# Optimization experiments

Hardware: AMD Instinct MI355X
Metric: run time of the kernel (lower is better)

Reference implementation:

```python
import jax, jax.numpy as jnp
import numpy as np

D_MODEL = 1024
ED = 2048          # d_inner = 2 * d_model
N = 16             # d_state
DT_RANK = 64
K = 4              # d_conv
BETA = 0.6
ALPHA = 1.0
B_SZ, L = 1, 2048


def setup_inputs() -> dict:
    key = jax.random.key(0)
    ks = jax.random.split(key, 9)
    s = 0.02
    x = jax.random.normal(ks[0], (B_SZ, L, D_MODEL), jnp.float32)
    W_in = jax.random.normal(ks[1], (2 * ED, D_MODEL), jnp.float32) * s
    conv_w = jax.random.normal(ks[2], (ED, K), jnp.float32) * s
    conv_b = jax.random.normal(ks[3], (ED,), jnp.float32) * s
    W_x = jax.random.normal(ks[4], (DT_RANK + 2 * N, ED), jnp.float32) * s
    dt_std = DT_RANK ** -0.5
    W_dt = jax.random.uniform(ks[5], (ED, DT_RANK), jnp.float32, -dt_std, dt_std)
    # dt bias init: inverse-softplus of dt in [dt_min, dt_max]
    dt = jnp.exp(jax.random.uniform(ks[6], (ED,), jnp.float32)
                 * (np.log(0.1) - np.log(0.001)) + np.log(0.001))
    dt = jnp.clip(dt, 1e-4)
    b_dt = dt + jnp.log(-jnp.expm1(-dt))
    A_log = jnp.log(jnp.tile(jnp.arange(1, N + 1, dtype=jnp.float32), (ED, 1)))
    D = jnp.ones((ED,), jnp.float32)
    W_out = jax.random.normal(ks[7], (D_MODEL, ED), jnp.float32) * s
    return {"x": x, "W_in": W_in, "conv_w": conv_w, "conv_b": conv_b,
            "W_x": W_x, "W_dt": W_dt, "b_dt": b_dt, "A_log": A_log,
            "D": D, "W_out": W_out}


def _depthwise_causal_conv(xc, conv_w, conv_b):
    # xc: (B, L, ED); torch Conv1d(groups=ED, padding=K-1)[..., :L] == causal conv
    lhs = jnp.transpose(xc, (0, 2, 1))                       # (B, ED, L)
    lhs = jnp.pad(lhs, ((0, 0), (0, 0), (K - 1, 0)))
    out = jax.lax.conv_general_dilated(lhs, conv_w[:, None, :], (1,), 'VALID',
                                       feature_group_count=ED)  # (B, ED, L)
    return jnp.transpose(out, (0, 2, 1)) + conv_b


def _ssm_momentum(xc, W_x, W_dt, b_dt, A_log, D):
    A = -jnp.exp(A_log)                                      # (ED, N)
    dBC = xc @ W_x.T                                         # (B, L, dt_rank + 2N)
    delta, Bm, Cm = jnp.split(dBC, [DT_RANK, DT_RANK + N], axis=-1)
    delta = jax.nn.softplus(delta @ W_dt.T + b_dt)           # (B, L, ED)
    deltaA = jnp.exp(delta[..., None] * A)                   # (B, L, ED, N)
    u = ALPHA * delta[..., None] * Bm[:, :, None, :] * xc[..., None]  # (B, L, ED, N)

    def step(carry, inp):
        h, v = carry
        dA_t, u_t = inp
        v = BETA * v + u_t
        h = dA_t * h + v
        return (h, v), h

    h0 = jnp.zeros((xc.shape[0], ED, N), xc.dtype)
    _, hs = jax.lax.scan(step, (h0, h0),
                         (jnp.moveaxis(deltaA, 1, 0), jnp.moveaxis(u, 1, 0)))
    y = jnp.einsum('lben,bln->ble', hs, Cm)                  # (B, L, ED)
    return y + D * xc


def reference(x, W_in, conv_w, conv_b, W_x, W_dt, b_dt, A_log, D, W_out):
    xz = x @ W_in.T                                          # (B, L, 2*ED)
    xc, z = jnp.split(xz, 2, axis=-1)
    xc = jax.nn.silu(_depthwise_causal_conv(xc, conv_w, conv_b))
    y = _ssm_momentum(xc, W_x, W_dt, b_dt, A_log, D)
    return (y * jax.nn.silu(z)) @ W_out.T                    # (B, L, d_model)
```

## Files before the change

### kernel.cpp

```cpp
#include <hip/hip_runtime.h>
#include <hip/hip_bf16.h>
#include <math.h>

#define L 2048
#define DM 1024
#define ED 2048
#define NST 16
#define DTR 64
#define BETA 0.6f
#define NCHUNK 64
#define LCH 32
#define SPLITS 16
#define SPLIT4 4

typedef __bf16 bf16_t;
typedef __bf16 bf16x8 __attribute__((ext_vector_type(8)));
typedef __bf16 bf16x4 __attribute__((ext_vector_type(4)));
typedef float  floatx4 __attribute__((ext_vector_type(4)));


__global__ void k_fill(float* __restrict__ p, float v, int n) {
    int i = blockIdx.x * 256 + threadIdx.x;
    if (i < n) p[i] = v;
}

__global__ void k_cvt_all(const float4* __restrict__ sx, bf16x4* __restrict__ dx,
                          const float4* __restrict__ s1, bf16x4* __restrict__ d1,
                          const float4* __restrict__ s2, bf16x4* __restrict__ d2,
                          const float4* __restrict__ s3, bf16x4* __restrict__ d3,
                          const float4* __restrict__ s4, bf16x4* __restrict__ d4) {
    int i = blockIdx.x * 256 + threadIdx.x;
    const float4* s; bf16x4* d; int off;
    if (i < 524288)        { s = sx; d = dx; off = 0; }
    else if (i < 1572864)  { s = s1; d = d1; off = 524288; }
    else if (i < 1622016)  { s = s2; d = d2; off = 1572864; }
    else if (i < 1654784)  { s = s3; d = d3; off = 1622016; }
    else                   { s = s4; d = d4; off = 1654784; }
    int j = i - off;
    float4 f = s[j];
    bf16x4 o;
    o[0] = (bf16_t)f.x; o[1] = (bf16_t)f.y; o[2] = (bf16_t)f.z; o[3] = (bf16_t)f.w;
    d[j] = o;
}

template<int EPI, bool GUARD>
__global__ __launch_bounds__(256)
void k_gemm_bt(const bf16_t* __restrict__ X, const bf16_t* __restrict__ W,
               float* __restrict__ C, int M, int N, int K, int ldc, int ksz,
               const float* __restrict__ bias) {
    __shared__ bf16_t As[128 * 32];
    __shared__ bf16_t Bs[128 * 32];
    const int tid  = threadIdx.x;
    const int bx   = blockIdx.x, by = blockIdx.y;
    const int kbase = blockIdx.z * ksz;
    if (EPI != 2) C += (size_t)blockIdx.z * M * ldc;
    const int wave = tid >> 6, lane = tid & 63;
    const int wm   = (wave >> 1) * 64;
    const int wn   = (wave & 1) * 64;
    const int quad = lane >> 4, l16 = lane & 15;

    floatx4 acc[4][4];
#pragma unroll
    for (int i = 0; i < 4; i++)
#pragma unroll
        for (int j = 0; j < 4; j++)
            acc[i][j] = (floatx4){0.f, 0.f, 0.f, 0.f};

    for (int kt = kbase; kt < kbase + ksz; kt += 32) {
        if (GUARD) {
#pragma unroll
            for (int p = 0; p < 2; p++) {
                int e = p * 2048 + tid * 8;
                int r = e >> 5, c = e & 31;
                int arow = by * 128 + r;
                *(float4*)(&As[r * 32 + c]) =
                    *(const float4*)(&X[(size_t)arow * K + kt + c]);
                int brow = bx * 128 + r;
                float4 bv = make_float4(0.f, 0.f, 0.f, 0.f);
                if (brow < N) bv = *(const float4*)(&W[(size_t)brow * K + kt + c]);
                *(float4*)(&Bs[r * 32 + c]) = bv;
            }
        } else {
#pragma unroll
            for (int p = 0; p < 2; p++) {
                int e = p * 2048 + tid * 8;
                int r = e >> 5, c = e & 31;
                __builtin_amdgcn_global_load_lds(
                    (const __attribute__((address_space(1))) void*)&X[(size_t)(by * 128 + r) * K + kt + c],
                    (__attribute__((address_space(3))) void*)&As[e], 16, 0, 0);
                __builtin_amdgcn_global_load_lds(
                    (const __attribute__((address_space(1))) void*)&W[(size_t)(bx * 128 + r) * K + kt + c],
                    (__attribute__((address_space(3))) void*)&Bs[e], 16, 0, 0);
            }
        }
        __syncthreads();

        bf16x8 af[4], bfr[4];
#pragma unroll
        for (int mt = 0; mt < 4; mt++)
            af[mt] = *(const bf16x8*)(&As[(wm + mt * 16 + l16) * 32 + quad * 8]);
#pragma unroll
        for (int nt = 0; nt < 4; nt++)
            bfr[nt] = *(const bf16x8*)(&Bs[(wn + nt * 16 + l16) * 32 + quad * 8]);
#pragma unroll
        for (int mt = 0; mt < 4; mt++)
#pragma unroll
            for (int nt = 0; nt < 4; nt++)
                acc[mt][nt] = __builtin_amdgcn_mfma_f32_16x16x32_bf16(
                    af[mt], bfr[nt], acc[mt][nt], 0, 0, 0);
        __syncthreads();
    }

#pragma unroll
    for (int mt = 0; mt < 4; mt++) {
#pragma unroll
        for (int nt = 0; nt < 4; nt++) {
            int col = bx * 128 + wn + nt * 16 + l16;
            if (!GUARD || col < N) {
#pragma unroll
                for (int r4 = 0; r4 < 4; r4++) {
                    int row = by * 128 + wm + mt * 16 + quad * 4 + r4;
                    float v = acc[mt][nt][r4];
                    if (EPI == 1) {
                        v += bias[col];
                        v = (v > 20.f) ? v : log1pf(__expf(v));
                    }
                    if (EPI == 2) {
                        unsafeAtomicAdd(&C[(size_t)row * ldc + col], v);
                    } else {
                        C[(size_t)row * ldc + col] = v;
                    }
                }
            }
        }
    }
}

__global__ void k_conv_silu(const float* __restrict__ xz,
                            const float* __restrict__ conv_w,
                            const float* __restrict__ conv_b,
                            float* __restrict__ xc, bf16_t* __restrict__ xc_bf) {
    int idx = blockIdx.x * 256 + threadIdx.x;
    int e = idx & (ED - 1);
    int t = idx >> 11;
    float w0 = conv_w[e * 4 + 0], w1 = conv_w[e * 4 + 1];
    float w2 = conv_w[e * 4 + 2], w3 = conv_w[e * 4 + 3];
    const float* col = xz + e;
    float acc = conv_b[e];
    if (t >= 3) acc += w0 * col[(size_t)(t - 3) * 4096];
    if (t >= 2) acc += w1 * col[(size_t)(t - 2) * 4096];
    if (t >= 1) acc += w2 * col[(size_t)(t - 1) * 4096];
    acc += w3 * col[(size_t)t * 4096];
    float s = acc / (1.f + __expf(-acc));
    xc[idx] = s;
    xc_bf[idx] = (bf16_t)s;
}

__global__ void k_red2(const float* __restrict__ part, float* __restrict__ dBC,
                       bf16_t* __restrict__ dly) {
    int idx = blockIdx.x * 256 + threadIdx.x;
    int t = idx / 96, c = idx - t * 96;
    float s = 0.f;
#pragma unroll
    for (int sp = 0; sp < SPLITS; sp++) s += part[(size_t)sp * L * 96 + idx];
    dBC[idx] = s;
    if (c < 64) dly[t * 64 + c] = (bf16_t)s;
}


__global__ __launch_bounds__(256)
void k_scan_p1(const float* __restrict__ delta, const float* __restrict__ xc,
               const float* __restrict__ dBC, const float* __restrict__ A_log,
               float4* __restrict__ summ) {
    const int chunk = blockIdx.x >> 3;
    const int e = (blockIdx.x & 7) * 256 + threadIdx.x;
    float A[NST];
#pragma unroll
    for (int n = 0; n < NST; n++) A[n] = -__expf(A_log[e * NST + n]);
    float h[NST], v[NST], p[NST], q[NST];
#pragma unroll
    for (int n = 0; n < NST; n++) { h[n] = 0.f; v[n] = 0.f; p[n] = 1.f; q[n] = 0.f; }
    float bp = 1.f;
    const int t0 = chunk * LCH;
    for (int i = 0; i < LCH; i++) {
        int t = t0 + i;
        float d   = delta[(size_t)t * ED + e];
        float xcv = xc[(size_t)t * ED + e];
        float du  = d * xcv;
        bp *= BETA;
        const float* Bp = &dBC[t * 96 + 64];
#pragma unroll
        for (int n = 0; n < NST; n++) {
            float a = __expf(d * A[n]);
            v[n] = BETA * v[n] + du * Bp[n];
            h[n] = a * h[n] + v[n];
            p[n] *= a;
            q[n] = a * q[n] + bp;
        }
    }
#pragma unroll
    for (int n = 0; n < NST; n++)
        summ[((size_t)n * NCHUNK + chunk) * ED + e] = make_float4(h[n], v[n], p[n], q[n]);
}

__global__ void k_combine(float4* __restrict__ summ) {
    int tid = blockIdx.x * 256 + threadIdx.x;
    int n = tid >> 11, e = tid & (ED - 1);
    float2* s2 = (float2*)summ;
    float h = 0.f, v = 0.f;
    const float bl = 7.9586611e-8f;
#pragma unroll 8
    for (int c = 0; c < NCHUNK; c++) {
        size_t idx = ((size_t)n * NCHUNK + c) * ED + e;
        float4 f = summ[idx];
        s2[idx * 2] = make_float2(h, v);
        float hn = f.z * h + f.w * v + f.x;
        v = bl * v + f.y;
        h = hn;
    }
}

__global__ __launch_bounds__(256)
void k_scan_p2(const float* __restrict__ delta, const float* __restrict__ xc,
               const float* __restrict__ dBC, const float* __restrict__ A_log,
               const float4* __restrict__ summ, const float* __restrict__ Dvec,
               const float* __restrict__ xz, bf16_t* __restrict__ g) {
    const int chunk = blockIdx.x >> 3;
    const int e = (blockIdx.x & 7) * 256 + threadIdx.x;
    float A[NST];
#pragma unroll
    for (int n = 0; n < NST; n++) A[n] = -__expf(A_log[e * NST + n]);
    float h[NST], v[NST];
    const float2* s2 = (const float2*)summ;
#pragma unroll
    for (int n = 0; n < NST; n++) {
        float2 s = s2[(((size_t)n * NCHUNK + chunk) * ED + e) * 2];
        h[n] = s.x; v[n] = s.y;
    }
    const float De = Dvec[e];
    const int t0 = chunk * LCH;
    for (int i = 0; i < LCH; i++) {
        int t = t0 + i;
        float d   = delta[(size_t)t * ED + e];
        float xcv = xc[(size_t)t * ED + e];
        float du  = d * xcv;
        const float* Bp = &dBC[t * 96 + 64];
        const float* Cp = &dBC[t * 96 + 80];
        float yacc = 0.f;
#pragma unroll
        for (int n = 0; n < NST; n++) {
            float a = __expf(d * A[n]);
            v[n] = BETA * v[n] + du * Bp[n];
            h[n] = a * h[n] + v[n];
            yacc += Cp[n] * h[n];
        }
        float z = xz[(size_t)t * 4096 + ED + e];
        float sz = z / (1.f + __expf(-z));
        g[(size_t)t * ED + e] = (bf16_t)((yacc + De * xcv) * sz);
    }
}


extern "C" void kernel_launch(void* const* d_in, const int* in_sizes, int n_in,
                              void* d_out, int out_size, void* d_ws, size_t ws_size,
                              hipStream_t stream) {
    const float* x      = (const float*)d_in[0];
    const float* W_in   = (const float*)d_in[1];
    const float* conv_w = (const float*)d_in[2];
    const float* conv_b = (const float*)d_in[3];
    const float* W_x    = (const float*)d_in[4];
    const float* W_dt   = (const float*)d_in[5];
    const float* b_dt   = (const float*)d_in[6];
    const float* A_log  = (const float*)d_in[7];
    const float* Dv     = (const float*)d_in[8];
    const float* W_out  = (const float*)d_in[9];
    float* out = (float*)d_out;

    constexpr size_t OFF_XZ    = 0;
    constexpr size_t OFF_XC    = 33554432;
    constexpr size_t OFF_C     = 50331648;
    constexpr size_t OFF_DELTA = 58720256;
    constexpr size_t OFF_R1    = 75497472;
    constexpr size_t OFF_XBF   = 109051904;
    constexpr size_t OFF_DBC   = 113246208;
    constexpr size_t OFF_DLY   = 114032640;
    constexpr size_t OFF_WX    = 114294784;
    constexpr size_t OFF_WDT   = 114688000;
    constexpr size_t OFF_WOUT  = 114950144;
    constexpr size_t WS_NEED   = 119144448;

    if (ws_size < WS_NEED) {
        k_fill<<<(out_size + 255) / 256, 256, 0, stream>>>(out, 1.0e9f, out_size);
        return;
    }

    char* ws = (char*)d_ws;
    float*  xz    = (float*)(ws + OFF_XZ);
    float*  xc    = (float*)(ws + OFF_XC);
    bf16_t* xc_bf = (bf16_t*)(ws + OFF_C);
    bf16_t* g_bf  = (bf16_t*)(ws + OFF_C);
    float*  delta = (float*)(ws + OFF_DELTA);
    bf16_t* Win_bf  = (bf16_t*)(ws + OFF_R1);
    float*  part2   = (float*)(ws + OFF_R1 + 16777216);
    float4* summ    = (float4*)(ws + OFF_R1);
    bf16_t* x_bf  = (bf16_t*)(ws + OFF_XBF);
    float*  dBC   = (float*)(ws + OFF_DBC);
    bf16_t* dly   = (bf16_t*)(ws + OFF_DLY);
    bf16_t* Wx_bf  = (bf16_t*)(ws + OFF_WX);
    bf16_t* Wdt_bf = (bf16_t*)(ws + OFF_WDT);
    bf16_t* Wout_bf = (bf16_t*)(ws + OFF_WOUT);

    k_cvt_all<<<2179072 / 256, 256, 0, stream>>>(
        (const float4*)x,     (bf16x4*)x_bf,
        (const float4*)W_in,  (bf16x4*)Win_bf,
        (const float4*)W_x,   (bf16x4*)Wx_bf,
        (const float4*)W_dt,  (bf16x4*)Wdt_bf,
        (const float4*)W_out, (bf16x4*)Wout_bf);

    hipMemsetAsync(out, 0, (size_t)out_size * sizeof(float), stream);

    {
        dim3 g(4096 / 128, L / 128, 1);
        k_gemm_bt<0, false><<<g, 256, 0, stream>>>(x_bf, Win_bf, xz, L, 4096, DM, 4096, DM, nullptr);
    }
    k_conv_silu<<<L * ED / 256, 256, 0, stream>>>(xz, conv_w, conv_b, xc, xc_bf);
    {
        dim3 g(1, L / 128, SPLITS);
        k_gemm_bt<0, true><<<g, 256, 0, stream>>>(xc_bf, Wx_bf, part2, L, 96, ED, 96, ED / SPLITS, nullptr);
    }
    k_red2<<<L * 96 / 256, 256, 0, stream>>>(part2, dBC, dly);
    {
        dim3 g(ED / 128, L / 128, 1);
        k_gemm_bt<1, false><<<g, 256, 0, stream>>>(dly, Wdt_bf, delta, L, ED, DTR, ED, DTR, b_dt);
    }
    k_scan_p1<<<NCHUNK * 8, 256, 0, stream>>>(delta, xc, dBC, A_log, summ);
    k_combine<<<ED * NST / 256, 256, 0, stream>>>(summ);
    k_scan_p2<<<NCHUNK * 8, 256, 0, stream>>>(delta, xc, dBC, A_log, summ, Dv, xz, g_bf);
    {
        dim3 g(DM / 128, L / 128, SPLIT4);
        k_gemm_bt<2, false><<<g, 256, 0, stream>>>(g_bf, Wout_bf, out, L, DM, ED, DM, ED / SPLIT4, nullptr);
    }
}
```

Baseline: 286.3 us.

## Split-K in-projection GEMM and replace atomic out-proj with partial buffers plus reduction

The in-projection GEMM now runs split-K over two halves, writing partials to separate workspace regions. The conv kernel sums both partials for the x half and folds the z half back into the main buffer. The output GEMM writes four plain partial slices instead of using float atomics, and a new kernel adds them into the output, which also drops the memset. This trades atomic contention and low in-projection parallelism for extra partial-buffer traffic and one more launch.

```diff
diff --git a/kernel.cpp b/kernel.cpp
--- a/kernel.cpp
+++ b/kernel.cpp
@@ -47,13 +47,13 @@
 __global__ __launch_bounds__(256)
 void k_gemm_bt(const bf16_t* __restrict__ X, const bf16_t* __restrict__ W,
                float* __restrict__ C, int M, int N, int K, int ldc, int ksz,
-               const float* __restrict__ bias) {
+               long pstride, const float* __restrict__ bias) {
     __shared__ bf16_t As[128 * 32];
     __shared__ bf16_t Bs[128 * 32];
     const int tid  = threadIdx.x;
     const int bx   = blockIdx.x, by = blockIdx.y;
     const int kbase = blockIdx.z * ksz;
-    if (EPI != 2) C += (size_t)blockIdx.z * M * ldc;
+    C += (size_t)blockIdx.z * pstride;
     const int wave = tid >> 6, lane = tid & 63;
     const int wm   = (wave >> 1) * 64;
     const int wn   = (wave & 1) * 64;
@@ -125,18 +125,23 @@
                         v += bias[col];
                         v = (v > 20.f) ? v : log1pf(__expf(v));
                     }
-                    if (EPI == 2) {
-                        unsafeAtomicAdd(&C[(size_t)row * ldc + col], v);
-                    } else {
-                        C[(size_t)row * ldc + col] = v;
-                    }
+                    C[(size_t)row * ldc + col] = v;
                 }
             }
         }
     }
 }
 
-__global__ void k_conv_silu(const float* __restrict__ xz,
+__global__ void k_red4(const float4* __restrict__ part, float4* __restrict__ out) {
+    int i = blockIdx.x * 256 + threadIdx.x;
+    const int stride = L * DM / 4;
+    float4 a = part[i], b = part[i + stride];
+    float4 c = part[i + 2 * stride], d = part[i + 3 * stride];
+    out[i] = make_float4(a.x + b.x + c.x + d.x, a.y + b.y + c.y + d.y,
+                         a.z + b.z + c.z + d.z, a.w + b.w + c.w + d.w);
+}
+
+__global__ void k_conv_silu(float* __restrict__ pA, const float* __restrict__ pB,
                             const float* __restrict__ conv_w,
                             const float* __restrict__ conv_b,
                             float* __restrict__ xc, bf16_t* __restrict__ xc_bf) {
@@ -145,15 +150,18 @@
     int t = idx >> 11;
     float w0 = conv_w[e * 4 + 0], w1 = conv_w[e * 4 + 1];
     float w2 = conv_w[e * 4 + 2], w3 = conv_w[e * 4 + 3];
-    const float* col = xz + e;
+    const float* colA = pA + e;
+    const float* colB = pB + e;
     float acc = conv_b[e];
-    if (t >= 3) acc += w0 * col[(size_t)(t - 3) * 4096];
-    if (t >= 2) acc += w1 * col[(size_t)(t - 2) * 4096];
-    if (t >= 1) acc += w2 * col[(size_t)(t - 1) * 4096];
-    acc += w3 * col[(size_t)t * 4096];
+    if (t >= 3) acc += w0 * (colA[(size_t)(t - 3) * 4096] + colB[(size_t)(t - 3) * 4096]);
+    if (t >= 2) acc += w1 * (colA[(size_t)(t - 2) * 4096] + colB[(size_t)(t - 2) * 4096]);
+    if (t >= 1) acc += w2 * (colA[(size_t)(t - 1) * 4096] + colB[(size_t)(t - 1) * 4096]);
+    acc += w3 * (colA[(size_t)t * 4096] + colB[(size_t)t * 4096]);
     float s = acc / (1.f + __expf(-acc));
     xc[idx] = s;
     xc_bf[idx] = (bf16_t)s;
+    size_t zi = (size_t)t * 4096 + ED + e;
+    pA[zi] = pA[zi] + pB[zi];
 }
 
 __global__ void k_red2(const float* __restrict__ part, float* __restrict__ dBC,
@@ -296,13 +304,15 @@
 
     char* ws = (char*)d_ws;
     float*  xz    = (float*)(ws + OFF_XZ);
+    float*  part4 = (float*)(ws + OFF_XZ);
     float*  xc    = (float*)(ws + OFF_XC);
     bf16_t* xc_bf = (bf16_t*)(ws + OFF_C);
     bf16_t* g_bf  = (bf16_t*)(ws + OFF_C);
-    float*  delta = (float*)(ws + OFF_DELTA);
-    bf16_t* Win_bf  = (bf16_t*)(ws + OFF_R1);
-    float*  part2   = (float*)(ws + OFF_R1 + 16777216);
-    float4* summ    = (float4*)(ws + OFF_R1);
+    bf16_t* Win_bf = (bf16_t*)(ws + OFF_DELTA);
+    float*  delta  = (float*)(ws + OFF_DELTA);
+    float*  partB  = (float*)(ws + OFF_R1);
+    float*  part2  = (float*)(ws + OFF_R1 + 16777216);
+    float4* summ   = (float4*)(ws + OFF_R1);
     bf16_t* x_bf  = (bf16_t*)(ws + OFF_XBF);
     float*  dBC   = (float*)(ws + OFF_DBC);
     bf16_t* dly   = (bf16_t*)(ws + OFF_DLY);
@@ -317,27 +327,30 @@
         (const float4*)W_dt,  (bf16x4*)Wdt_bf,
         (const float4*)W_out, (bf16x4*)Wout_bf);
 
-    hipMemsetAsync(out, 0, (size_t)out_size * sizeof(float), stream);
-
     {
-        dim3 g(4096 / 128, L / 128, 1);
-        k_gemm_bt<0, false><<<g, 256, 0, stream>>>(x_bf, Win_bf, xz, L, 4096, DM, 4096, DM, nullptr);
-    }
-    k_conv_silu<<<L * ED / 256, 256, 0, stream>>>(xz, conv_w, conv_b, xc, xc_bf);
+        dim3 g(4096 / 128, L / 128, 2);
+        k_gemm_bt<0, false><<<g, 256, 0, stream>>>(x_bf, Win_bf, xz, L, 4096, DM,
+                                                   4096, DM / 2, (long)(OFF_R1 / 4), nullptr);
+    }
+    k_conv_silu<<<L * ED / 256, 256, 0, stream>>>(xz, partB, conv_w, conv_b, xc, xc_bf);
     {
         dim3 g(1, L / 128, SPLITS);
-        k_gemm_bt<0, true><<<g, 256, 0, stream>>>(xc_bf, Wx_bf, part2, L, 96, ED, 96, ED / SPLITS, nullptr);
+        k_gemm_bt<0, true><<<g, 256, 0, stream>>>(xc_bf, Wx_bf, part2, L, 96, ED,
+                                                  96, ED / SPLITS, (long)L * 96, nullptr);
     }
     k_red2<<<L * 96 / 256, 256, 0, stream>>>(part2, dBC, dly);
     {
         dim3 g(ED / 128, L / 128, 1);
-        k_gemm_bt<1, false><<<g, 256, 0, stream>>>(dly, Wdt_bf, delta, L, ED, DTR, ED, DTR, b_dt);
+        k_gemm_bt<1, false><<<g, 256, 0, stream>>>(dly, Wdt_bf, delta, L, ED, DTR,
+                                                   ED, DTR, 0L, b_dt);
     }
     k_scan_p1<<<NCHUNK * 8, 256, 0, stream>>>(delta, xc, dBC, A_log, summ);
     k_combine<<<ED * NST / 256, 256, 0, stream>>>(summ);
     k_scan_p2<<<NCHUNK * 8, 256, 0, stream>>>(delta, xc, dBC, A_log, summ, Dv, xz, g_bf);
     {
         dim3 g(DM / 128, L / 128, SPLIT4);
-        k_gemm_bt<2, false><<<g, 256, 0, stream>>>(g_bf, Wout_bf, out, L, DM, ED, DM, ED / SPLIT4, nullptr);
-    }
-}
+        k_gemm_bt<0, false><<<g, 256, 0, stream>>>(g_bf, Wout_bf, part4, L, DM, ED,
+                                                   DM, ED / SPLIT4, (long)L * DM, nullptr);
+    }
+    k_red4<<<L * DM / 4 / 256, 256, 0, stream>>>((const float4*)part4, (float4*)out);
+}
```

After: 284.2 us. About the same (-0.7%).
